# Optimization experiments

Measured on AMD Instinct MI355X. Metric: run time of the kernel, lower is better.

## Reference

```python
import jax, jax.numpy as jnp
import numpy as np
import math

B, N, C, H, CH = 4, 1024, 512, 8, 64  # batch, seq (Q=K), model dim, heads, head dim

def setup_inputs() -> dict:
    key = jax.random.key(0)
    ks = jax.random.split(key, 11)
    s = 0.02  # small init scale for weights
    f32 = jnp.float32
    return {
        "q_x": jax.random.normal(ks[0], (B, N, C), f32),
        "kv_x": jax.random.normal(ks[1], (B, N, C), f32),
        "bias_mask": jax.random.normal(ks[2], (B, 1, 1, N), f32),
        "bias_pair": jax.random.normal(ks[3], (1, H, N, N), f32),
        "Wq": (jax.random.normal(ks[4], (C, H * CH), f32) * s),
        "Wk": (jax.random.normal(ks[5], (C, H * CH), f32) * s),
        "Wv": (jax.random.normal(ks[6], (C, H * CH), f32) * s),
        "Wg": (jax.random.normal(ks[7], (C, H * CH), f32) * s),
        "bg": jnp.ones((H * CH,), f32),           # 'gating' init: bias=1
        "Wo": (jax.random.normal(ks[8], (H * CH, C), f32) * s),
        "bo": jnp.zeros((C,), f32),               # 'final' init
    }

def reference(q_x, kv_x, bias_mask, bias_pair, Wq, Wk, Wv, Wg, bg, Wo, bo):
    inv_sqrt = 1.0 / math.sqrt(CH)
    # projections -> [B, N, H, CH]
    q = (q_x @ Wq).reshape(B, N, H, CH) * inv_sqrt
    k = (kv_x @ Wk).reshape(B, N, H, CH)
    v = (kv_x @ Wv).reshape(B, N, H, CH)
    # scores [B, H, Q, K] with additive broadcast biases
    scores = jnp.einsum("bqhc,bkhc->bhqk", q, k) + bias_mask + bias_pair
    a = jax.nn.softmax(scores, axis=-1)
    o = jnp.einsum("bhqk,bkhc->bqhc", a, v)  # [B, Q, H, CH]
    # gated output
    g = jax.nn.sigmoid(q_x @ Wg + bg).reshape(B, N, H, CH)
    o = o * g
    out = o.reshape(B, N, H * CH) @ Wo + bo  # [B, Q, C]
    return out
```

## Files before the change

### kernel.cpp

```cpp
#include <hip/hip_runtime.h>
#include <hip/hip_bf16.h>
#include <hip/hip_fp16.h>

#define B_ 4
#define N_ 1024
#define C_ 512
#define H_ 8
#define CH_ 64

typedef _Float16 f16x8 __attribute__((ext_vector_type(8)));
typedef _Float16 f16x4 __attribute__((ext_vector_type(4)));
typedef float f32x4 __attribute__((ext_vector_type(4)));

__global__ void cvt_f32_f16(const float* __restrict__ xq, const float* __restrict__ xkv,
                            _Float16* __restrict__ oq, _Float16* __restrict__ okv) {
  const int n4 = (B_ * N_ * C_) / 4;
  int stride = gridDim.x * blockDim.x;
  for (int idx = blockIdx.x * blockDim.x + threadIdx.x; idx < 2 * n4; idx += stride) {
    const float4* src = (idx < n4) ? (const float4*)xq : (const float4*)xkv;
    _Float16* dst = (idx < n4) ? oq : okv;
    int j = (idx < n4) ? idx : idx - n4;
    float4 v = src[j];
    f16x4 h;
    h[0] = (_Float16)v.x; h[1] = (_Float16)v.y;
    h[2] = (_Float16)v.z; h[3] = (_Float16)v.w;
    *(f16x4*)(dst + (size_t)j * 4) = h;
  }
}

__global__ void transpose_w(const float* __restrict__ Wq, const float* __restrict__ Wk,
                            const float* __restrict__ Wv, const float* __restrict__ Wg,
                            const float* __restrict__ Wo, _Float16* __restrict__ WT) {
  int s = blockIdx.z;
  const float* W = (s == 0) ? Wq : (s == 1) ? Wk : (s == 2) ? Wv : (s == 3) ? Wg : Wo;
  __shared__ float tile[32][33];
  int tx = threadIdx.x & 31, ty = threadIdx.x >> 5;
  int k0 = blockIdx.x * 32, n0 = blockIdx.y * 32;
  #pragma unroll
  for (int r = 0; r < 32; r += 8)
    tile[ty + r][tx] = W[(size_t)(k0 + ty + r) * C_ + n0 + tx];
  __syncthreads();
  _Float16* dst = WT + (size_t)s * C_ * C_;
  #pragma unroll
  for (int r = 0; r < 32; r += 8)
    dst[(size_t)(n0 + ty + r) * C_ + k0 + tx] = (_Float16)tile[tx][ty + r];
}

__global__ __launch_bounds__(256, 2) void proj_gemm(
    const _Float16* __restrict__ xq16, const _Float16* __restrict__ xkv16,
    const _Float16* __restrict__ WT, const float* __restrict__ bg,
    _Float16* __restrict__ Qb, _Float16* __restrict__ Kb,
    _Float16* __restrict__ Vt, _Float16* __restrict__ Gb) {
  int nt0 = blockIdx.x * 128;
  int m0 = blockIdx.y * 128;
  int sel = nt0 >> 9;
  int n0 = nt0 & 511;
  const _Float16* X = (sel == 0 || sel == 3) ? xq16 : xkv16;
  const _Float16* Wt = WT + (size_t)sel * C_ * C_;

  __shared__ __align__(16) char lds[32768];
  char* ldsA = lds;
  char* ldsB = lds + 16384;

  int tid = threadIdx.x;
  int lane = tid & 63, w = tid >> 6;
  int wr = w >> 1, wc = w & 1;
  int lr = lane & 15, lg = lane >> 4;

  f32x4 acc[4][4];
  #pragma unroll
  for (int i = 0; i < 4; i++)
    #pragma unroll
    for (int j = 0; j < 4; j++)
      #pragma unroll
      for (int r = 0; r < 4; r++) acc[i][j][r] = 0.f;

  int srow = tid >> 3, scol = tid & 7;

  for (int k0 = 0; k0 < C_; k0 += 64) {
    __syncthreads();
    #pragma unroll
    for (int p = 0; p < 4; p++) {
      int r = p * 32 + srow;
      *(f16x8*)(ldsA + ((r * 128 + scol * 16) ^ ((r & 7) << 4))) =
          *(const f16x8*)(X + (size_t)(m0 + r) * C_ + k0 + scol * 8);
      *(f16x8*)(ldsB + ((r * 128 + scol * 16) ^ ((r & 7) << 4))) =
          *(const f16x8*)(Wt + (size_t)(n0 + r) * C_ + k0 + scol * 8);
    }
    __syncthreads();
    #pragma unroll
    for (int kh = 0; kh < 2; kh++) {
      f16x8 a[4], b[4];
      #pragma unroll
      for (int i = 0; i < 4; i++) {
        int row = wr * 64 + i * 16 + lr;
        a[i] = *(const f16x8*)(ldsA + ((row * 128 + kh * 64 + lg * 16) ^ ((row & 7) << 4)));
        int col = wc * 64 + i * 16 + lr;
        b[i] = *(const f16x8*)(ldsB + ((col * 128 + kh * 64 + lg * 16) ^ ((col & 7) << 4)));
      }
      #pragma unroll
      for (int i = 0; i < 4; i++)
        #pragma unroll
        for (int j = 0; j < 4; j++)
          acc[i][j] = __builtin_amdgcn_mfma_f32_16x16x32_f16(a[i], b[j], acc[i][j], 0, 0, 0);
    }
  }

  const float inv_sqrt = 0.125f;
  #pragma unroll
  for (int i = 0; i < 4; i++) {
    int token = m0 + wr * 64 + i * 16 + lg * 4;
    #pragma unroll
    for (int j = 0; j < 4; j++) {
      int col = n0 + wc * 64 + j * 16 + lr;
      f32x4 v = acc[i][j];
      if (sel == 0) {
        #pragma unroll
        for (int r = 0; r < 4; r++)
          Qb[(size_t)(token + r) * C_ + col] = (_Float16)(v[r] * inv_sqrt);
      } else if (sel == 1) {
        #pragma unroll
        for (int r = 0; r < 4; r++)
          Kb[(size_t)(token + r) * C_ + col] = (_Float16)v[r];
      } else if (sel == 2) {
        int bb = token >> 10;
        int nn = token & 1023;
        int hh = col >> 6, ch = col & 63;
        f16x4 pk;
        #pragma unroll
        for (int r = 0; r < 4; r++) pk[r] = (_Float16)v[r];
        *(f16x4*)(Vt + (size_t)((bb * H_ + hh) * CH_ + ch) * N_ + nn) = pk;
      } else {
        #pragma unroll
        for (int r = 0; r < 4; r++) {
          float x = v[r] + bg[col];
          Gb[(size_t)(token + r) * C_ + col] = (_Float16)(1.f / (1.f + __expf(-x)));
        }
      }
    }
  }
}

__global__ __launch_bounds__(256, 2) void attn(
    const _Float16* __restrict__ Qb, const _Float16* __restrict__ Kb,
    const _Float16* __restrict__ Vt, const _Float16* __restrict__ Gb,
    const float* __restrict__ bias_mask, const float* __restrict__ bias_pair,
    _Float16* __restrict__ Ob) {
  int bid = blockIdx.x;
  int h = bid & 7, b = (bid >> 3) & 3, qt = bid >> 5;
  int q0 = qt * 64;
  int tid = threadIdx.x, lane = tid & 63, w = tid >> 6;
  int lr = lane & 15, lg = lane >> 4;

  __shared__ __align__(16) char lds[49152];
  char* ldsK = lds;
  char* ldsV = lds + 16384;
  char* ldsP = lds + 32768;

  f16x8 qf[2];
  {
    int token = b * N_ + q0 + w * 16 + lr;
    const _Float16* qp = Qb + (size_t)token * C_ + h * CH_;
    qf[0] = *(const f16x8*)(qp + lg * 8);
    qf[1] = *(const f16x8*)(qp + 32 + lg * 8);
  }

  f32x4 acc_o[4];
  #pragma unroll
  for (int j = 0; j < 4; j++)
    #pragma unroll
    for (int r = 0; r < 4; r++) acc_o[j][r] = 0.f;
  float m_run = -1e30f, l_run = 0.f;

  int srow = tid >> 3, scol = tid & 7;
  int vrow = tid >> 4, vcol = tid & 15;

  const _Float16* Kbase = Kb + (size_t)(b * N_) * C_ + h * CH_;
  const _Float16* Vbase = Vt + (size_t)((b * H_ + h) * CH_) * N_;

  f16x8 kr[4], vr[4];
  #pragma unroll
  for (int p = 0; p < 4; p++) {
    kr[p] = *(const f16x8*)(Kbase + (size_t)(p * 32 + srow) * C_ + scol * 8);
    vr[p] = *(const f16x8*)(Vbase + (size_t)(p * 16 + vrow) * N_ + vcol * 8);
  }

  for (int kt = 0; kt < 8; kt++) {
    __syncthreads();
    #pragma unroll
    for (int p = 0; p < 4; p++) {
      int r = p * 32 + srow;
      *(f16x8*)(ldsK + ((r * 128 + scol * 16) ^ ((r & 7) << 4))) = kr[p];
      int rv = p * 16 + vrow;
      *(f16x8*)(ldsV + ((rv * 256 + vcol * 16) ^ ((rv & 7) << 4))) = vr[p];
    }
    __syncthreads();
    if (kt < 7) {
      #pragma unroll
      for (int p = 0; p < 4; p++) {
        kr[p] = *(const f16x8*)(Kbase + (size_t)((kt + 1) * 128 + p * 32 + srow) * C_ + scol * 8);
        vr[p] = *(const f16x8*)(Vbase + (size_t)(p * 16 + vrow) * N_ + (kt + 1) * 128 + vcol * 8);
      }
    }
    f32x4 bias[8];
    {
      const float* bp = bias_pair + ((size_t)h * N_ + q0 + w * 16 + lr) * N_ + kt * 128 + lg * 4;
      const float* bm = bias_mask + b * N_ + kt * 128 + lg * 4;
      #pragma unroll
      for (int ct = 0; ct < 8; ct++)
        bias[ct] = *(const f32x4*)(bp + ct * 16) + *(const f32x4*)(bm + ct * 16);
    }
    f32x4 s[8];
    #pragma unroll
    for (int ct = 0; ct < 8; ct++) {
      #pragma unroll
      for (int r = 0; r < 4; r++) s[ct][r] = 0.f;
      #pragma unroll
      for (int kh = 0; kh < 2; kh++) {
        int row = ct * 16 + lr;
        f16x8 kf = *(const f16x8*)(ldsK + ((row * 128 + kh * 64 + lg * 16) ^ ((row & 7) << 4)));
        s[ct] = __builtin_amdgcn_mfma_f32_16x16x32_f16(kf, qf[kh], s[ct], 0, 0, 0);
      }
      s[ct] += bias[ct];
    }
    float mx = s[0][0];
    #pragma unroll
    for (int ct = 0; ct < 8; ct++)
      #pragma unroll
      for (int r = 0; r < 4; r++) mx = fmaxf(mx, s[ct][r]);
    mx = fmaxf(mx, __shfl_xor(mx, 16, 64));
    mx = fmaxf(mx, __shfl_xor(mx, 32, 64));
    float m_new = fmaxf(m_run, mx);
    float sc = __expf(m_run - m_new);
    m_run = m_new;
    float sum = 0.f;
    #pragma unroll
    for (int ct = 0; ct < 8; ct++)
      #pragma unroll
      for (int r = 0; r < 4; r++) {
        float p = __expf(s[ct][r] - m_new);
        s[ct][r] = p;
        sum += p;
      }
    sum += __shfl_xor(sum, 16, 64);
    sum += __shfl_xor(sum, 32, 64);
    l_run = l_run * sc + sum;
    #pragma unroll
    for (int j = 0; j < 4; j++)
      #pragma unroll
      for (int r = 0; r < 4; r++) acc_o[j][r] *= sc;
    char* myP = ldsP + w * 4096;
    #pragma unroll
    for (int ct = 0; ct < 8; ct++) {
      f16x4 pk;
      #pragma unroll
      for (int r = 0; r < 4; r++) pk[r] = (_Float16)s[ct][r];
      *(f16x4*)(myP + ((lr * 256 + ct * 32 + lg * 8) ^ ((lr & 7) << 4))) = pk;
    }
    #pragma unroll
    for (int ks = 0; ks < 4; ks++) {
      f16x8 pf = *(const f16x8*)(myP + ((lr * 256 + ks * 64 + lg * 16) ^ ((lr & 7) << 4)));
      #pragma unroll
      for (int cc = 0; cc < 4; cc++) {
        int vrr = cc * 16 + lr;
        f16x8 vf = *(const f16x8*)(ldsV + ((vrr * 256 + ks * 64 + lg * 16) ^ ((vrr & 7) << 4)));
        acc_o[cc] = __builtin_amdgcn_mfma_f32_16x16x32_f16(vf, pf, acc_o[cc], 0, 0, 0);
      }
    }
  }

  {
    int token = b * N_ + q0 + w * 16 + lr;
    float inv_l = 1.f / l_run;
    #pragma unroll
    for (int cc = 0; cc < 4; cc++) {
      int col = h * CH_ + cc * 16 + lg * 4;
      f16x4 g4 = *(const f16x4*)(Gb + (size_t)token * C_ + col);
      f16x4 o4;
      #pragma unroll
      for (int r = 0; r < 4; r++)
        o4[r] = (_Float16)(acc_o[cc][r] * inv_l * (float)g4[r]);
      *(f16x4*)(Ob + (size_t)token * C_ + col) = o4;
    }
  }
}

__global__ __launch_bounds__(256, 2) void out_gemm(
    const _Float16* __restrict__ Ob, const _Float16* __restrict__ WTo,
    const float* __restrict__ bo, float* __restrict__ out) {
  int n0 = blockIdx.x * 128;
  int m0 = blockIdx.y * 128;
  __shared__ __align__(16) char lds[32768];
  char* ldsA = lds;
  char* ldsB = lds + 16384;
  int tid = threadIdx.x;
  int lane = tid & 63, w = tid >> 6;
  int wr = w >> 1, wc = w & 1;
  int lr = lane & 15, lg = lane >> 4;
  f32x4 acc[4][4];
  #pragma unroll
  for (int i = 0; i < 4; i++)
    #pragma unroll
    for (int j = 0; j < 4; j++)
      #pragma unroll
      for (int r = 0; r < 4; r++) acc[i][j][r] = 0.f;
  int srow = tid >> 3, scol = tid & 7;
  for (int k0 = 0; k0 < C_; k0 += 64) {
    __syncthreads();
    #pragma unroll
    for (int p = 0; p < 4; p++) {
      int r = p * 32 + srow;
      *(f16x8*)(ldsA + ((r * 128 + scol * 16) ^ ((r & 7) << 4))) =
          *(const f16x8*)(Ob + (size_t)(m0 + r) * C_ + k0 + scol * 8);
      *(f16x8*)(ldsB + ((r * 128 + scol * 16) ^ ((r & 7) << 4))) =
          *(const f16x8*)(WTo + (size_t)(n0 + r) * C_ + k0 + scol * 8);
    }
    __syncthreads();
    #pragma unroll
    for (int kh = 0; kh < 2; kh++) {
      f16x8 a[4], bfr[4];
      #pragma unroll
      for (int i = 0; i < 4; i++) {
        int row = wr * 64 + i * 16 + lr;
        a[i] = *(const f16x8*)(ldsA + ((row * 128 + kh * 64 + lg * 16) ^ ((row & 7) << 4)));
        int col = wc * 64 + i * 16 + lr;
        bfr[i] = *(const f16x8*)(ldsB + ((col * 128 + kh * 64 + lg * 16) ^ ((col & 7) << 4)));
      }
      #pragma unroll
      for (int i = 0; i < 4; i++)
        #pragma unroll
        for (int j = 0; j < 4; j++)
          acc[i][j] = __builtin_amdgcn_mfma_f32_16x16x32_f16(a[i], bfr[j], acc[i][j], 0, 0, 0);
    }
  }
  #pragma unroll
  for (int i = 0; i < 4; i++) {
    int token = m0 + wr * 64 + i * 16 + lg * 4;
    #pragma unroll
    for (int j = 0; j < 4; j++) {
      int col = n0 + wc * 64 + j * 16 + lr;
      float bb = bo[col];
      #pragma unroll
      for (int r = 0; r < 4; r++)
        out[(size_t)(token + r) * C_ + col] = acc[i][j][r] + bb;
    }
  }
}

extern "C" void kernel_launch(void* const* d_in, const int* in_sizes, int n_in,
                              void* d_out, int out_size, void* d_ws, size_t ws_size,
                              hipStream_t stream) {
  const float* q_x = (const float*)d_in[0];
  const float* kv_x = (const float*)d_in[1];
  const float* bias_mask = (const float*)d_in[2];
  const float* bias_pair = (const float*)d_in[3];
  const float* Wq = (const float*)d_in[4];
  const float* Wk = (const float*)d_in[5];
  const float* Wv = (const float*)d_in[6];
  const float* Wg = (const float*)d_in[7];
  const float* bg = (const float*)d_in[8];
  const float* Wo = (const float*)d_in[9];
  const float* bo = (const float*)d_in[10];
  float* out = (float*)d_out;

  char* ws = (char*)d_ws;
  const size_t MB = 1024 * 1024;
  _Float16* xq16 = (_Float16*)(ws + 0);
  _Float16* xkv16 = (_Float16*)(ws + 4 * MB);
  _Float16* WT = (_Float16*)(ws + 8 * MB);
  _Float16* Qb = (_Float16*)(ws + 11 * MB);
  _Float16* Kb = (_Float16*)(ws + 15 * MB);
  _Float16* Vt = (_Float16*)(ws + 19 * MB);
  _Float16* Gb = (_Float16*)(ws + 23 * MB);
  _Float16* Ob = (_Float16*)(ws + 31 * MB);

  cvt_f32_f16<<<2048, 256, 0, stream>>>(q_x, kv_x, xq16, xkv16);
  transpose_w<<<dim3(16, 16, 5), 256, 0, stream>>>(Wq, Wk, Wv, Wg, Wo, WT);
  proj_gemm<<<dim3(16, 32), 256, 0, stream>>>(xq16, xkv16, WT, bg, Qb, Kb, Vt, Gb);
  attn<<<512, 256, 0, stream>>>(Qb, Kb, Vt, Gb, bias_mask, bias_pair, Ob);
  out_gemm<<<dim3(4, 32), 256, 0, stream>>>(Ob, WT + 4 * (size_t)C_ * C_, bo, out);
}
```

Before: 77.21 us.

## Split attention over two key halves with a separate merge-and-gate kernel

The attention kernel now splits the key dimension into two halves (split-K / flash-decoding style), doubling the grid to 1024 blocks. Each block writes an unnormalized partial output plus its running max and sum, and a new merge_gate kernel combines the two halves, normalizes, and applies the sigmoid gate. It also drops the LDS round trip for P by feeding the softmax registers straight into 16x16x16 MFMAs, shrinks LDS, raises the occupancy hint, and folds the bias into the accumulator init. The cost is an extra kernel launch and extra global traffic for partials, with the buffers reusing workspace regions.

```diff
diff --git a/kernel.cpp b/kernel.cpp
--- a/kernel.cpp
+++ b/kernel.cpp
@@ -141,21 +141,20 @@
   }
 }
 
-__global__ __launch_bounds__(256, 2) void attn(
+__global__ __launch_bounds__(256, 4) void attn(
     const _Float16* __restrict__ Qb, const _Float16* __restrict__ Kb,
-    const _Float16* __restrict__ Vt, const _Float16* __restrict__ Gb,
+    const _Float16* __restrict__ Vt,
     const float* __restrict__ bias_mask, const float* __restrict__ bias_pair,
-    _Float16* __restrict__ Ob) {
+    _Float16* __restrict__ Opart, float* __restrict__ ml) {
   int bid = blockIdx.x;
-  int h = bid & 7, b = (bid >> 3) & 3, qt = bid >> 5;
+  int h = bid & 7, b = (bid >> 3) & 3, p = (bid >> 5) & 1, qt = bid >> 6;
   int q0 = qt * 64;
   int tid = threadIdx.x, lane = tid & 63, w = tid >> 6;
   int lr = lane & 15, lg = lane >> 4;
 
-  __shared__ __align__(16) char lds[49152];
+  __shared__ __align__(16) char lds[32768];
   char* ldsK = lds;
   char* ldsV = lds + 16384;
-  char* ldsP = lds + 32768;
 
   f16x8 qf[2];
   {
@@ -175,53 +174,48 @@
   int srow = tid >> 3, scol = tid & 7;
   int vrow = tid >> 4, vcol = tid & 15;
 
-  const _Float16* Kbase = Kb + (size_t)(b * N_) * C_ + h * CH_;
-  const _Float16* Vbase = Vt + (size_t)((b * H_ + h) * CH_) * N_;
+  const _Float16* Kbase = Kb + ((size_t)(b * N_ + p * 512)) * C_ + h * CH_;
+  const _Float16* Vbase = Vt + (size_t)((b * H_ + h) * CH_) * N_ + p * 512;
+  const float* bpbase = bias_pair + ((size_t)h * N_ + q0 + w * 16 + lr) * N_ + p * 512 + lg * 4;
+  const float* bmbase = bias_mask + b * N_ + p * 512 + lg * 4;
 
   f16x8 kr[4], vr[4];
   #pragma unroll
-  for (int p = 0; p < 4; p++) {
-    kr[p] = *(const f16x8*)(Kbase + (size_t)(p * 32 + srow) * C_ + scol * 8);
-    vr[p] = *(const f16x8*)(Vbase + (size_t)(p * 16 + vrow) * N_ + vcol * 8);
-  }
-
-  for (int kt = 0; kt < 8; kt++) {
-    __syncthreads();
-    #pragma unroll
-    for (int p = 0; p < 4; p++) {
-      int r = p * 32 + srow;
-      *(f16x8*)(ldsK + ((r * 128 + scol * 16) ^ ((r & 7) << 4))) = kr[p];
-      int rv = p * 16 + vrow;
-      *(f16x8*)(ldsV + ((rv * 256 + vcol * 16) ^ ((rv & 7) << 4))) = vr[p];
-    }
-    __syncthreads();
-    if (kt < 7) {
-      #pragma unroll
-      for (int p = 0; p < 4; p++) {
-        kr[p] = *(const f16x8*)(Kbase + (size_t)((kt + 1) * 128 + p * 32 + srow) * C_ + scol * 8);
-        vr[p] = *(const f16x8*)(Vbase + (size_t)(p * 16 + vrow) * N_ + (kt + 1) * 128 + vcol * 8);
-      }
-    }
-    f32x4 bias[8];
-    {
-      const float* bp = bias_pair + ((size_t)h * N_ + q0 + w * 16 + lr) * N_ + kt * 128 + lg * 4;
-      const float* bm = bias_mask + b * N_ + kt * 128 + lg * 4;
-      #pragma unroll
-      for (int ct = 0; ct < 8; ct++)
-        bias[ct] = *(const f32x4*)(bp + ct * 16) + *(const f32x4*)(bm + ct * 16);
+  for (int pp = 0; pp < 4; pp++) {
+    kr[pp] = *(const f16x8*)(Kbase + (size_t)(pp * 32 + srow) * C_ + scol * 8);
+    vr[pp] = *(const f16x8*)(Vbase + (size_t)(pp * 16 + vrow) * N_ + vcol * 8);
+  }
+
+  for (int kt = 0; kt < 4; kt++) {
+    __syncthreads();
+    #pragma unroll
+    for (int pp = 0; pp < 4; pp++) {
+      int r = pp * 32 + srow;
+      *(f16x8*)(ldsK + ((r * 128 + scol * 16) ^ ((r & 7) << 4))) = kr[pp];
+      int rv = pp * 16 + vrow;
+      *(f16x8*)(ldsV + ((rv * 256 + vcol * 16) ^ ((rv & 7) << 4))) = vr[pp];
+    }
+    __syncthreads();
+    if (kt < 3) {
+      #pragma unroll
+      for (int pp = 0; pp < 4; pp++) {
+        kr[pp] = *(const f16x8*)(Kbase + (size_t)((kt + 1) * 128 + pp * 32 + srow) * C_ + scol * 8);
+        vr[pp] = *(const f16x8*)(Vbase + (size_t)(pp * 16 + vrow) * N_ + (kt + 1) * 128 + vcol * 8);
+      }
     }
     f32x4 s[8];
     #pragma unroll
+    for (int ct = 0; ct < 8; ct++)
+      s[ct] = *(const f32x4*)(bpbase + kt * 128 + ct * 16) +
+              *(const f32x4*)(bmbase + kt * 128 + ct * 16);
+    #pragma unroll
     for (int ct = 0; ct < 8; ct++) {
-      #pragma unroll
-      for (int r = 0; r < 4; r++) s[ct][r] = 0.f;
       #pragma unroll
       for (int kh = 0; kh < 2; kh++) {
         int row = ct * 16 + lr;
         f16x8 kf = *(const f16x8*)(ldsK + ((row * 128 + kh * 64 + lg * 16) ^ ((row & 7) << 4)));
         s[ct] = __builtin_amdgcn_mfma_f32_16x16x32_f16(kf, qf[kh], s[ct], 0, 0, 0);
       }
-      s[ct] += bias[ct];
     }
     float mx = s[0][0];
     #pragma unroll
@@ -238,9 +232,9 @@
     for (int ct = 0; ct < 8; ct++)
       #pragma unroll
       for (int r = 0; r < 4; r++) {
-        float p = __expf(s[ct][r] - m_new);
-        s[ct][r] = p;
-        sum += p;
+        float pv = __expf(s[ct][r] - m_new);
+        s[ct][r] = pv;
+        sum += pv;
       }
     sum += __shfl_xor(sum, 16, 64);
     sum += __shfl_xor(sum, 32, 64);
@@ -249,39 +243,67 @@
     for (int j = 0; j < 4; j++)
       #pragma unroll
       for (int r = 0; r < 4; r++) acc_o[j][r] *= sc;
-    char* myP = ldsP + w * 4096;
     #pragma unroll
     for (int ct = 0; ct < 8; ct++) {
-      f16x4 pk;
-      #pragma unroll
-      for (int r = 0; r < 4; r++) pk[r] = (_Float16)s[ct][r];
-      *(f16x4*)(myP + ((lr * 256 + ct * 32 + lg * 8) ^ ((lr & 7) << 4))) = pk;
-    }
-    #pragma unroll
-    for (int ks = 0; ks < 4; ks++) {
-      f16x8 pf = *(const f16x8*)(myP + ((lr * 256 + ks * 64 + lg * 16) ^ ((lr & 7) << 4)));
+      f16x4 pf;
+      #pragma unroll
+      for (int r = 0; r < 4; r++) pf[r] = (_Float16)s[ct][r];
       #pragma unroll
       for (int cc = 0; cc < 4; cc++) {
         int vrr = cc * 16 + lr;
-        f16x8 vf = *(const f16x8*)(ldsV + ((vrr * 256 + ks * 64 + lg * 16) ^ ((vrr & 7) << 4)));
-        acc_o[cc] = __builtin_amdgcn_mfma_f32_16x16x32_f16(vf, pf, acc_o[cc], 0, 0, 0);
+        f16x4 vf = *(const f16x4*)(ldsV + ((vrr * 256 + ct * 32 + lg * 8) ^ ((vrr & 7) << 4)));
+        acc_o[cc] = __builtin_amdgcn_mfma_f32_16x16x16f16(vf, pf, acc_o[cc], 0, 0, 0);
       }
     }
   }
 
   {
-    int token = b * N_ + q0 + w * 16 + lr;
-    float inv_l = 1.f / l_run;
+    _Float16* Op = Opart + (size_t)bid * 4096;
+    int qq = w * 16 + lr;
     #pragma unroll
     for (int cc = 0; cc < 4; cc++) {
-      int col = h * CH_ + cc * 16 + lg * 4;
-      f16x4 g4 = *(const f16x4*)(Gb + (size_t)token * C_ + col);
       f16x4 o4;
       #pragma unroll
-      for (int r = 0; r < 4; r++)
-        o4[r] = (_Float16)(acc_o[cc][r] * inv_l * (float)g4[r]);
-      *(f16x4*)(Ob + (size_t)token * C_ + col) = o4;
-    }
+      for (int r = 0; r < 4; r++) o4[r] = (_Float16)acc_o[cc][r];
+      *(f16x4*)(Op + qq * 64 + cc * 16 + lg * 4) = o4;
+    }
+    if (lg == 0) {
+      float2 v; v.x = m_run; v.y = l_run;
+      *(float2*)(ml + (size_t)(bid * 64 + qq) * 2) = v;
+    }
+  }
+}
+
+__global__ __launch_bounds__(256) void merge_gate(
+    const _Float16* __restrict__ Opart, const float* __restrict__ ml,
+    const _Float16* __restrict__ Gb, _Float16* __restrict__ Ob) {
+  int mbid = blockIdx.x;
+  int h = mbid & 7, b = (mbid >> 3) & 3, qt = mbid >> 5;
+  int tid = threadIdx.x;
+  int qrow = tid >> 2, ch0 = (tid & 3) * 16;
+  int bid0 = h + b * 8 + qt * 64;
+  int bid1 = bid0 + 32;
+  float2 ml0 = *(const float2*)(ml + (size_t)(bid0 * 64 + qrow) * 2);
+  float2 ml1 = *(const float2*)(ml + (size_t)(bid1 * 64 + qrow) * 2);
+  float M = fmaxf(ml0.x, ml1.x);
+  float e0 = __expf(ml0.x - M), e1 = __expf(ml1.x - M);
+  float inv = 1.f / (e0 * ml0.y + e1 * ml1.y);
+  e0 *= inv; e1 *= inv;
+  int token = b * N_ + qt * 64 + qrow;
+  const _Float16* O0 = Opart + (size_t)bid0 * 4096 + qrow * 64 + ch0;
+  const _Float16* O1 = Opart + (size_t)bid1 * 4096 + qrow * 64 + ch0;
+  const _Float16* G = Gb + (size_t)token * C_ + h * CH_ + ch0;
+  _Float16* Od = Ob + (size_t)token * C_ + h * CH_ + ch0;
+  #pragma unroll
+  for (int t = 0; t < 2; t++) {
+    f16x8 a0 = *(const f16x8*)(O0 + t * 8);
+    f16x8 a1 = *(const f16x8*)(O1 + t * 8);
+    f16x8 g8 = *(const f16x8*)(G + t * 8);
+    f16x8 o8;
+    #pragma unroll
+    for (int j = 0; j < 8; j++)
+      o8[j] = (_Float16)(((float)a0[j] * e0 + (float)a1[j] * e1) * (float)g8[j]);
+    *(f16x8*)(Od + t * 8) = o8;
   }
 }
 
@@ -367,16 +389,19 @@
   const size_t MB = 1024 * 1024;
   _Float16* xq16 = (_Float16*)(ws + 0);
   _Float16* xkv16 = (_Float16*)(ws + 4 * MB);
+  _Float16* Opart = (_Float16*)(ws + 0);
   _Float16* WT = (_Float16*)(ws + 8 * MB);
   _Float16* Qb = (_Float16*)(ws + 11 * MB);
   _Float16* Kb = (_Float16*)(ws + 15 * MB);
   _Float16* Vt = (_Float16*)(ws + 19 * MB);
   _Float16* Gb = (_Float16*)(ws + 23 * MB);
-  _Float16* Ob = (_Float16*)(ws + 31 * MB);
+  _Float16* Ob = (_Float16*)(ws + 27 * MB);
+  float* ml = (float*)(ws + 31 * MB);
 
   cvt_f32_f16<<<2048, 256, 0, stream>>>(q_x, kv_x, xq16, xkv16);
   transpose_w<<<dim3(16, 16, 5), 256, 0, stream>>>(Wq, Wk, Wv, Wg, Wo, WT);
   proj_gemm<<<dim3(16, 32), 256, 0, stream>>>(xq16, xkv16, WT, bg, Qb, Kb, Vt, Gb);
-  attn<<<512, 256, 0, stream>>>(Qb, Kb, Vt, Gb, bias_mask, bias_pair, Ob);
+  attn<<<1024, 256, 0, stream>>>(Qb, Kb, Vt, bias_mask, bias_pair, Opart, ml);
+  merge_gate<<<512, 256, 0, stream>>>(Opart, ml, Gb, Ob);
   out_gemm<<<dim3(4, 32), 256, 0, stream>>>(Ob, WT + 4 * (size_t)C_ * C_, bo, out);
 }
```

Result: slower. 122.3 us (+58.4%).
